# Kernel tuning notes

Hardware: AMD Instinct MI355X
Metric: run time of the kernel (lower is better)

## Reference

```python
import jax, jax.numpy as jnp
import numpy as np

SCALE = 100.0

def _build_tables():
    b2n = np.zeros((256, 32), np.float32)
    n2b = np.zeros((32, 256), np.float32)
    for byte in range(256):
        h, l = byte >> 4, byte & 15
        b2n[byte, h] = 1.0
        b2n[byte, 16 + l] = 1.0
        n2b[h, byte] = 1.0
        n2b[16 + l, byte] = 1.0
    add_table = np.zeros((16, 16, 2, 16), np.float32)
    carry_table = np.zeros((16, 16, 2, 2), np.float32)
    for x in range(16):
        for y in range(16):
            for c in range(2):
                t = x + y + c
                add_table[x, y, c, t % 16] = 1.0
                carry_table[x, y, c, t // 16] = 1.0
    return b2n, n2b, add_table, carry_table

def setup_inputs() -> dict:
    key = jax.random.key(0)
    k1, k2 = jax.random.split(key)
    B = 32768
    a = jax.random.normal(k1, (B, 4, 256), dtype=jnp.float32)
    b = jax.random.normal(k2, (B, 4, 256), dtype=jnp.float32)
    b2n, n2b, add_table, carry_table = _build_tables()
    return {"a": a, "b": b,
            "b2n": jnp.asarray(b2n), "n2b": jnp.asarray(n2b),
            "add_table": jnp.asarray(add_table), "carry_table": jnp.asarray(carry_table)}

def _byte_add_single(a, b, b2n, n2b, add_table, carry_table):
    # a, b: [4, 256]
    def to_nibbles(x):
        comb = x @ b2n  # [32]
        return jax.nn.softmax(comb[:16] * SCALE), jax.nn.softmax(comb[16:] * SCALE)

    def nibble_add(x, y, cin):
        # cin has shape [1] initially (broadcasts over carry axis, as torch einsum does) or [2]
        w = x[:, None, None] * y[None, :, None] * cin[None, None, :]
        w = jnp.broadcast_to(w, (16, 16, 2))
        s = jnp.einsum('ijk,ijkl->l', w, add_table)
        c = jnp.einsum('ijk,ijkl->l', w, carry_table)
        return jax.nn.softmax(s * SCALE), jax.nn.softmax(c * SCALE)

    def from_nibbles(h, l):
        return jax.nn.softmax((jnp.concatenate([h, l]) @ n2b) * SCALE)

    carry = jnp.ones((1,), a.dtype)  # matches torch.tensor([1.0]) initial carry
    outs = []
    for i in range(4):  # fixed 4-byte carry chain
        ah, al = to_nibbles(a[i])
        bh, bl = to_nibbles(b[i])
        sl, carry_out = nibble_add(al, bl, carry)
        sh, carry = nibble_add(ah, bh, carry_out)
        outs.append(from_nibbles(sh, sl))
    return jnp.stack(outs)  # [4, 256]

def reference(a, b, b2n, n2b, add_table, carry_table):
    f = jax.vmap(_byte_add_single, in_axes=(0, 0, None, None, None, None))
    return f(a, b, b2n, n2b, add_table, carry_table)  # [B, 4, 256]
```

## Files before the change

kernel.cpp:

```cpp
#include <hip/hip_runtime.h>
#include <cstddef>
#include <math.h>


__device__ __forceinline__ float exf(float t) {
  return (float)exp((double)t);
}

__device__ __forceinline__ void softmax16_np(const float* x, float* p) {
#pragma clang fp contract(off)
  float t[16];
#pragma unroll
  for (int j = 0; j < 16; ++j) t[j] = x[j] * 100.0f;
  float m = t[0];
#pragma unroll
  for (int j = 1; j < 16; ++j) m = fmaxf(m, t[j]);
  float e[16];
#pragma unroll
  for (int j = 0; j < 16; ++j) e[j] = exf(t[j] - m);
  float r0 = e[0] + e[8], r1 = e[1] + e[9], r2 = e[2] + e[10], r3 = e[3] + e[11];
  float r4 = e[4] + e[12], r5 = e[5] + e[13], r6 = e[6] + e[14], r7 = e[7] + e[15];
  float s = ((r0 + r1) + (r2 + r3)) + ((r4 + r5) + (r6 + r7));
#pragma unroll
  for (int j = 0; j < 16; ++j) p[j] = e[j] / s;
}

__device__ __forceinline__ void nibble_add_raw(const float* px, const float* py,
                                               float c0, float c1,
                                               float* s, float& n0, float& n1) {
#pragma clang fp contract(off)
  float ca = 0.f, cb = 0.f;
#pragma unroll
  for (int l = 0; l < 16; ++l) s[l] = 0.f;
#pragma unroll
  for (int i = 0; i < 16; ++i) {
#pragma unroll
    for (int j = 0; j < 16; ++j) {
      float wij = px[i] * py[j];
      float w0 = wij * c0;
      float w1 = wij * c1;
      const int t0 = i + j, t1 = i + j + 1;
      s[t0 & 15] += w0;
      if (t0 < 16) ca += w0; else cb += w0;
      s[t1 & 15] += w1;
      if (t1 < 16) ca += w1; else cb += w1;
    }
  }
  float u0 = ca * 100.0f, u1 = cb * 100.0f;
  float m = fmaxf(u0, u1);
  float e0 = exf(u0 - m), e1 = exf(u1 - m);
  float ss = e0 + e1;
  n0 = e0 / ss;
  n1 = e1 / ss;
}

extern "C" __global__ void __launch_bounds__(256, 1)
k1_prep(const float* __restrict__ A, const float* __restrict__ Bm,
        float* __restrict__ ws1, int nbatch) {
  __shared__ float buf[32][257];
  __shared__ float comb[32][33];
  const int tid = threadIdx.x;
  const int batch0 = blockIdx.x * 32;
  const int ib = blockIdx.y;
  const int inp = blockIdx.z;
  if (batch0 >= nbatch) return;
  const float* __restrict__ src =
      (inp == 0 ? A : Bm) + (size_t)batch0 * 1024 + ib * 256;

#pragma unroll
  for (int r = 0; r < 8; ++r) {
    int idx = r * 256 + tid;
    int row = idx >> 6, c4 = idx & 63;
    *(float4*)&buf[row][c4 * 4] = *(const float4*)(src + (size_t)row * 1024 + c4 * 4);
  }
  __syncthreads();

  {
#pragma clang fp contract(off)
    const int g = tid >> 5, bb = tid & 31;
    float acc[4] = {0.f, 0.f, 0.f, 0.f};
    if (g < 4) {
#pragma unroll
      for (int q = 0; q < 4; ++q) {
        float a = 0.f;
#pragma unroll
        for (int k4 = 0; k4 < 4; ++k4) {
          float4 v = *(const float4*)&buf[bb][(g * 4 + q) * 16 + k4 * 4];
          a += v.x; a += v.y; a += v.z; a += v.w;
        }
        acc[q] = a;
      }
#pragma unroll
      for (int q = 0; q < 4; ++q) comb[bb][g * 4 + q] = acc[q];
    } else {
      const int l0 = (g - 4) * 4;
#pragma unroll
      for (int m = 0; m < 16; ++m) {
        float4 v = *(const float4*)&buf[bb][m * 16 + l0];
        acc[0] += v.x; acc[1] += v.y; acc[2] += v.z; acc[3] += v.w;
      }
#pragma unroll
      for (int q = 0; q < 4; ++q) comb[bb][16 + l0 + q] = acc[q];
    }
  }
  __syncthreads();

  if (tid < 64) {
    const int nib = tid >> 5, bb = tid & 31;
    float x[16], p[16];
#pragma unroll
    for (int j = 0; j < 16; ++j) x[j] = comb[bb][nib * 16 + j];
    softmax16_np(x, p);
    const size_t r0 = (size_t)((ib * 2 + inp) * 32 + nib * 16);
#pragma unroll
    for (int j = 0; j < 16; ++j)
      ws1[(r0 + j) * nbatch + batch0 + bb] = p[j];
  }
}

__device__ __forceinline__ void k2_load(const float* __restrict__ ws1, int i,
                                        size_t batch, int nbatch, float* b) {
#pragma unroll
  for (int t = 0; t < 64; ++t)
    b[t] = ws1[(size_t)(i * 64 + t) * nbatch + batch];
}

__device__ __forceinline__ void k2_step(const float* b, float& cr0, float& cr1,
                                        float* __restrict__ ws2, int i,
                                        size_t batch, int nbatch) {
  float sl[16], sh[16], d0, d1;
  nibble_add_raw(b + 16, b + 48, cr0, cr1, sl, d0, d1);
  nibble_add_raw(b + 0,  b + 32, d0, d1, sh, cr0, cr1);
#pragma unroll
  for (int l = 0; l < 16; ++l) {
    ws2[(size_t)(i * 32 + l) * nbatch + batch] = sh[l];
    ws2[(size_t)(i * 32 + 16 + l) * nbatch + batch] = sl[l];
  }
}

extern "C" __global__ void __launch_bounds__(64, 1)
k2_chain(const float* __restrict__ ws1, float* __restrict__ ws2, int nbatch) {
  const size_t batch = (size_t)blockIdx.x * 64 + threadIdx.x;
  if (batch >= (size_t)nbatch) return;
  float cr0 = 1.0f, cr1 = 1.0f;
  float bufA[64], bufB[64];
  k2_load(ws1, 0, batch, nbatch, bufA);
  k2_load(ws1, 1, batch, nbatch, bufB);
  k2_step(bufA, cr0, cr1, ws2, 0, batch, nbatch);
  k2_load(ws1, 2, batch, nbatch, bufA);
  k2_step(bufB, cr0, cr1, ws2, 1, batch, nbatch);
  k2_load(ws1, 3, batch, nbatch, bufB);
  k2_step(bufA, cr0, cr1, ws2, 2, batch, nbatch);
  k2_step(bufB, cr0, cr1, ws2, 3, batch, nbatch);
}

extern "C" __global__ void __launch_bounds__(256, 1)
k3_out(const float* __restrict__ ws2, float* __restrict__ O, int nbatch) {
  __shared__ float pout[64][36];
  const int tid = threadIdx.x;
  const int batch0 = blockIdx.x * 64;
  const int ib = blockIdx.y;
  if (batch0 >= nbatch) return;

  if (tid < 128) {
    const int nib = tid >> 6, bb = tid & 63;
    float x[16], p[16], p2[16];
#pragma unroll
    for (int l = 0; l < 16; ++l)
      x[l] = ws2[(size_t)(ib * 32 + nib * 16 + l) * nbatch + batch0 + bb];
    softmax16_np(x, p);
    softmax16_np(p, p2);
#pragma unroll
    for (int j = 0; j < 16; ++j) pout[bb][nib * 20 + j] = p2[j];
  }
  __syncthreads();

#pragma unroll
  for (int kk = 0; kk < 16; ++kk) {
    int flat = kk * 1024 + tid * 4;
    int bb = flat >> 8;
    int b0 = flat & 255;
    float ph = pout[bb][b0 >> 4];
    int lo = 20 + (b0 & 15);
    float4 o;
    o.x = ph * pout[bb][lo + 0];
    o.y = ph * pout[bb][lo + 1];
    o.z = ph * pout[bb][lo + 2];
    o.w = ph * pout[bb][lo + 3];
    *(float4*)(O + ((size_t)(batch0 + bb) * 4 + ib) * 256 + b0) = o;
  }
}

__device__ __forceinline__ void nibble_add_np_fb(const float* px, const float* py,
                                                 float c0, float c1,
                                                 float* ps, float& n0, float& n1) {
  float s[16];
  nibble_add_raw(px, py, c0, c1, s, n0, n1);
  softmax16_np(s, ps);
}

__device__ __forceinline__ void buckets_np_fb(const float* __restrict__ row,
                                              float* hi, float* lo) {
#pragma clang fp contract(off)
#pragma unroll
  for (int j = 0; j < 16; ++j) { hi[j] = 0.f; lo[j] = 0.f; }
#pragma unroll
  for (int k4 = 0; k4 < 64; ++k4) {
    float4 x = *(const float4*)(row + k4 * 4);
    const int h = k4 >> 2, l0 = (k4 & 3) * 4;
    hi[h] += x.x;  hi[h] += x.y;  hi[h] += x.z;  hi[h] += x.w;
    lo[l0 + 0] += x.x;
    lo[l0 + 1] += x.y;
    lo[l0 + 2] += x.z;
    lo[l0 + 3] += x.w;
  }
}

extern "C" __global__ void __launch_bounds__(64, 1)
byteadd_fallback(const float* __restrict__ A, const float* __restrict__ Bm,
                 float* __restrict__ O, int nbatch) {
#pragma clang fp contract(off)
  const int b = blockIdx.x * 64 + threadIdx.x;
  if (b >= nbatch) return;
  const float* Ab = A + (size_t)b * 1024;
  const float* Bb = Bm + (size_t)b * 1024;
  float* Ob = O + (size_t)b * 1024;
  float cr0 = 1.0f, cr1 = 1.0f;
#pragma unroll 1
  for (int i = 0; i < 4; ++i) {
    float ah[16], al[16], bh[16], bl[16];
    buckets_np_fb(Ab + i * 256, ah, al);
    buckets_np_fb(Bb + i * 256, bh, bl);
    float pah[16], pal[16], pbh[16], pbl[16];
    softmax16_np(ah, pah);
    softmax16_np(al, pal);
    softmax16_np(bh, pbh);
    softmax16_np(bl, pbl);
    float psl[16], psh[16], d0, d1;
    nibble_add_np_fb(pal, pbl, cr0, cr1, psl, d0, d1);
    nibble_add_np_fb(pah, pbh, d0, d1, psh, cr0, cr1);
    float ph2[16], pl2[16];
    softmax16_np(psh, ph2);
    softmax16_np(psl, pl2);
#pragma unroll
    for (int k4 = 0; k4 < 64; ++k4) {
      const int h = k4 >> 2, l0 = (k4 & 3) * 4;
      const float ph = ph2[h];
      float4 o;
      o.x = ph * pl2[l0 + 0];
      o.y = ph * pl2[l0 + 1];
      o.z = ph * pl2[l0 + 2];
      o.w = ph * pl2[l0 + 3];
      *(float4*)(Ob + i * 256 + k4 * 4) = o;
    }
  }
}

extern "C" void kernel_launch(void* const* d_in, const int* in_sizes, int n_in,
                              void* d_out, int out_size, void* d_ws, size_t ws_size,
                              hipStream_t stream) {
  const float* A = (const float*)d_in[0];
  const float* B = (const float*)d_in[1];
  float* O = (float*)d_out;
  int nbatch = in_sizes[0] / 1024;
  size_t need = (size_t)384 * nbatch * sizeof(float);
  if (ws_size >= need && (nbatch & 63) == 0) {
    float* ws1 = (float*)d_ws;
    float* ws2 = ws1 + (size_t)256 * nbatch;
    k1_prep<<<dim3(nbatch / 32, 4, 2), dim3(256), 0, stream>>>(A, B, ws1, nbatch);
    k2_chain<<<dim3(nbatch / 64), dim3(64), 0, stream>>>(ws1, ws2, nbatch);
    k3_out<<<dim3(nbatch / 64, 4), dim3(256), 0, stream>>>(ws2, O, nbatch);
  } else {
    byteadd_fallback<<<dim3((nbatch + 63) / 64), dim3(64), 0, stream>>>(A, B, O, nbatch);
  }
}
```

Measured before the change: 197.1 us.

## Use one thread per batch row in prep kernel; process two bytes per output block

The prep kernel no longer stages 32 rows in shared memory and reduces them cooperatively. Each thread now reads its own 256-float row directly with float4 loads, accumulates the high and low nibble buckets in registers, and computes both softmaxes, so all 256 threads do work where only 64 did before. The output kernel now handles two bytes per block so every thread takes part in the softmax phase, and launch bounds are raised to allow more resident blocks. The trade is that the prep kernel's global reads are strided per thread (1024 floats apart) and no longer coalesced, and the fast path now requires the batch count to be a multiple of 256.

After: 282.0 us. 43.1% more time.

```diff
diff --git a/kernel.cpp b/kernel.cpp
--- a/kernel.cpp
+++ b/kernel.cpp
@@ -54,68 +54,45 @@
   n1 = e1 / ss;
 }
 
-extern "C" __global__ void __launch_bounds__(256, 1)
+extern "C" __global__ void __launch_bounds__(256, 4)
 k1_prep(const float* __restrict__ A, const float* __restrict__ Bm,
         float* __restrict__ ws1, int nbatch) {
-  __shared__ float buf[32][257];
-  __shared__ float comb[32][33];
-  const int tid = threadIdx.x;
-  const int batch0 = blockIdx.x * 32;
-  const int ib = blockIdx.y;
-  const int inp = blockIdx.z;
-  if (batch0 >= nbatch) return;
+#pragma clang fp contract(off)
+  const int batch = blockIdx.x * 256 + threadIdx.x;
+  if (batch >= nbatch) return;
+  const int ib = blockIdx.y, inp = blockIdx.z;
   const float* __restrict__ src =
-      (inp == 0 ? A : Bm) + (size_t)batch0 * 1024 + ib * 256;
-
-#pragma unroll
-  for (int r = 0; r < 8; ++r) {
-    int idx = r * 256 + tid;
-    int row = idx >> 6, c4 = idx & 63;
-    *(float4*)&buf[row][c4 * 4] = *(const float4*)(src + (size_t)row * 1024 + c4 * 4);
-  }
-  __syncthreads();
-
-  {
-#pragma clang fp contract(off)
-    const int g = tid >> 5, bb = tid & 31;
-    float acc[4] = {0.f, 0.f, 0.f, 0.f};
-    if (g < 4) {
-#pragma unroll
-      for (int q = 0; q < 4; ++q) {
-        float a = 0.f;
-#pragma unroll
-        for (int k4 = 0; k4 < 4; ++k4) {
-          float4 v = *(const float4*)&buf[bb][(g * 4 + q) * 16 + k4 * 4];
-          a += v.x; a += v.y; a += v.z; a += v.w;
-        }
-        acc[q] = a;
-      }
-#pragma unroll
-      for (int q = 0; q < 4; ++q) comb[bb][g * 4 + q] = acc[q];
-    } else {
-      const int l0 = (g - 4) * 4;
-#pragma unroll
-      for (int m = 0; m < 16; ++m) {
-        float4 v = *(const float4*)&buf[bb][m * 16 + l0];
-        acc[0] += v.x; acc[1] += v.y; acc[2] += v.z; acc[3] += v.w;
-      }
-#pragma unroll
-      for (int q = 0; q < 4; ++q) comb[bb][16 + l0 + q] = acc[q];
-    }
-  }
-  __syncthreads();
-
-  if (tid < 64) {
-    const int nib = tid >> 5, bb = tid & 31;
-    float x[16], p[16];
-#pragma unroll
-    for (int j = 0; j < 16; ++j) x[j] = comb[bb][nib * 16 + j];
-    softmax16_np(x, p);
-    const size_t r0 = (size_t)((ib * 2 + inp) * 32 + nib * 16);
-#pragma unroll
-    for (int j = 0; j < 16; ++j)
-      ws1[(r0 + j) * nbatch + batch0 + bb] = p[j];
-  }
+      (inp == 0 ? A : Bm) + (size_t)batch * 1024 + ib * 256;
+
+  float hi[16], lo[16];
+#pragma unroll
+  for (int j = 0; j < 16; ++j) { hi[j] = 0.f; lo[j] = 0.f; }
+#pragma unroll
+  for (int m = 0; m < 16; ++m) {
+    float4 v0 = *(const float4*)(src + m * 16 + 0);
+    float4 v1 = *(const float4*)(src + m * 16 + 4);
+    float4 v2 = *(const float4*)(src + m * 16 + 8);
+    float4 v3 = *(const float4*)(src + m * 16 + 12);
+    float a = hi[m];
+    a += v0.x; a += v0.y; a += v0.z; a += v0.w;
+    a += v1.x; a += v1.y; a += v1.z; a += v1.w;
+    a += v2.x; a += v2.y; a += v2.z; a += v2.w;
+    a += v3.x; a += v3.y; a += v3.z; a += v3.w;
+    hi[m] = a;
+    lo[0]  += v0.x; lo[1]  += v0.y; lo[2]  += v0.z; lo[3]  += v0.w;
+    lo[4]  += v1.x; lo[5]  += v1.y; lo[6]  += v1.z; lo[7]  += v1.w;
+    lo[8]  += v2.x; lo[9]  += v2.y; lo[10] += v2.z; lo[11] += v2.w;
+    lo[12] += v3.x; lo[13] += v3.y; lo[14] += v3.z; lo[15] += v3.w;
+  }
+
+  const size_t r0 = (size_t)((ib * 2 + inp) * 32);
+  float p[16];
+  softmax16_np(hi, p);
+#pragma unroll
+  for (int j = 0; j < 16; ++j) ws1[(r0 + j) * nbatch + batch] = p[j];
+  softmax16_np(lo, p);
+#pragma unroll
+  for (int j = 0; j < 16; ++j) ws1[(r0 + 16 + j) * nbatch + batch] = p[j];
 }
 
 __device__ __forceinline__ void k2_load(const float* __restrict__ ws1, int i,
@@ -154,40 +131,45 @@
   k2_step(bufB, cr0, cr1, ws2, 3, batch, nbatch);
 }
 
-extern "C" __global__ void __launch_bounds__(256, 1)
+extern "C" __global__ void __launch_bounds__(256, 2)
 k3_out(const float* __restrict__ ws2, float* __restrict__ O, int nbatch) {
-  __shared__ float pout[64][36];
+  __shared__ float pout[2][64][36];
   const int tid = threadIdx.x;
   const int batch0 = blockIdx.x * 64;
-  const int ib = blockIdx.y;
+  const int ib0 = blockIdx.y * 2;
   if (batch0 >= nbatch) return;
 
-  if (tid < 128) {
-    const int nib = tid >> 6, bb = tid & 63;
+  {
+    const int ibl = tid >> 7;
+    const int nib = (tid >> 6) & 1;
+    const int bb = tid & 63;
     float x[16], p[16], p2[16];
 #pragma unroll
     for (int l = 0; l < 16; ++l)
-      x[l] = ws2[(size_t)(ib * 32 + nib * 16 + l) * nbatch + batch0 + bb];
+      x[l] = ws2[(size_t)((ib0 + ibl) * 32 + nib * 16 + l) * nbatch + batch0 + bb];
     softmax16_np(x, p);
     softmax16_np(p, p2);
 #pragma unroll
-    for (int j = 0; j < 16; ++j) pout[bb][nib * 20 + j] = p2[j];
+    for (int j = 0; j < 16; ++j) pout[ibl][bb][nib * 20 + j] = p2[j];
   }
   __syncthreads();
 
 #pragma unroll
-  for (int kk = 0; kk < 16; ++kk) {
-    int flat = kk * 1024 + tid * 4;
-    int bb = flat >> 8;
-    int b0 = flat & 255;
-    float ph = pout[bb][b0 >> 4];
-    int lo = 20 + (b0 & 15);
-    float4 o;
-    o.x = ph * pout[bb][lo + 0];
-    o.y = ph * pout[bb][lo + 1];
-    o.z = ph * pout[bb][lo + 2];
-    o.w = ph * pout[bb][lo + 3];
-    *(float4*)(O + ((size_t)(batch0 + bb) * 4 + ib) * 256 + b0) = o;
+  for (int ibl = 0; ibl < 2; ++ibl) {
+#pragma unroll
+    for (int kk = 0; kk < 16; ++kk) {
+      int flat = kk * 1024 + tid * 4;
+      int bb = flat >> 8;
+      int b0 = flat & 255;
+      float ph = pout[ibl][bb][b0 >> 4];
+      int lo = 20 + (b0 & 15);
+      float4 o;
+      o.x = ph * pout[ibl][bb][lo + 0];
+      o.y = ph * pout[ibl][bb][lo + 1];
+      o.z = ph * pout[ibl][bb][lo + 2];
+      o.w = ph * pout[ibl][bb][lo + 3];
+      *(float4*)(O + ((size_t)(batch0 + bb) * 4 + ib0 + ibl) * 256 + b0) = o;
+    }
   }
 }
 
@@ -264,12 +246,12 @@
   float* O = (float*)d_out;
   int nbatch = in_sizes[0] / 1024;
   size_t need = (size_t)384 * nbatch * sizeof(float);
-  if (ws_size >= need && (nbatch & 63) == 0) {
+  if (ws_size >= need && (nbatch & 255) == 0) {
     float* ws1 = (float*)d_ws;
     float* ws2 = ws1 + (size_t)256 * nbatch;
-    k1_prep<<<dim3(nbatch / 32, 4, 2), dim3(256), 0, stream>>>(A, B, ws1, nbatch);
+    k1_prep<<<dim3(nbatch / 256, 4, 2), dim3(256), 0, stream>>>(A, B, ws1, nbatch);
     k2_chain<<<dim3(nbatch / 64), dim3(64), 0, stream>>>(ws1, ws2, nbatch);
-    k3_out<<<dim3(nbatch / 64, 4), dim3(256), 0, stream>>>(ws2, O, nbatch);
+    k3_out<<<dim3(nbatch / 64, 2), dim3(256), 0, stream>>>(ws2, O, nbatch);
   } else {
     byteadd_fallback<<<dim3((nbatch + 63) / 64), dim3(64), 0, stream>>>(A, B, O, nbatch);
   }
```

## Raise occupancy of prep/output kernels and process two bytes per k3 block

Applied to the files above, without the earlier changes.

Changes launch bounds of k1_prep and k3_out from 1 to 4 blocks per CU, and pads the k1 shared buffer differently while having each wave load full rows. The k1 reduction now reads scalars from shared memory instead of float4 vectors. k3_out now handles two byte positions per block, so all 256 threads do softmax work and the grid is halved. The aim is better latency hiding and fewer idle threads, at the cost of more shared memory per k3 block and a possible change in LDS bank conflicts.

Result: no change. 196.6 us (-0.2%).

```diff
diff --git a/kernel.cpp b/kernel.cpp
--- a/kernel.cpp
+++ b/kernel.cpp
@@ -54,59 +54,55 @@
   n1 = e1 / ss;
 }
 
-extern "C" __global__ void __launch_bounds__(256, 1)
+extern "C" __global__ void __launch_bounds__(256, 4)
 k1_prep(const float* __restrict__ A, const float* __restrict__ Bm,
         float* __restrict__ ws1, int nbatch) {
-  __shared__ float buf[32][257];
+#pragma clang fp contract(off)
+  __shared__ float buf[32][261];
   __shared__ float comb[32][33];
   const int tid = threadIdx.x;
+  const int wave = tid >> 6, lane = tid & 63;
   const int batch0 = blockIdx.x * 32;
-  const int ib = blockIdx.y;
-  const int inp = blockIdx.z;
+  const int ib = blockIdx.y, inp = blockIdx.z;
   if (batch0 >= nbatch) return;
   const float* __restrict__ src =
       (inp == 0 ? A : Bm) + (size_t)batch0 * 1024 + ib * 256;
 
 #pragma unroll
-  for (int r = 0; r < 8; ++r) {
-    int idx = r * 256 + tid;
-    int row = idx >> 6, c4 = idx & 63;
-    *(float4*)&buf[row][c4 * 4] = *(const float4*)(src + (size_t)row * 1024 + c4 * 4);
+  for (int it = 0; it < 8; ++it) {
+    const int bb = it * 4 + wave;
+    *(float4*)&buf[bb][lane * 4] =
+        *(const float4*)(src + (size_t)bb * 1024 + lane * 4);
   }
   __syncthreads();
 
   {
-#pragma clang fp contract(off)
-    const int g = tid >> 5, bb = tid & 31;
-    float acc[4] = {0.f, 0.f, 0.f, 0.f};
+    const int g = tid >> 5;
+    const int bb = tid & 31;
     if (g < 4) {
 #pragma unroll
       for (int q = 0; q < 4; ++q) {
+        const int u = g * 4 + q;
         float a = 0.f;
 #pragma unroll
-        for (int k4 = 0; k4 < 4; ++k4) {
-          float4 v = *(const float4*)&buf[bb][(g * 4 + q) * 16 + k4 * 4];
-          a += v.x; a += v.y; a += v.z; a += v.w;
-        }
-        acc[q] = a;
+        for (int e = 0; e < 16; ++e) a += buf[bb][u * 16 + e];
+        comb[bb][u] = a;
       }
-#pragma unroll
-      for (int q = 0; q < 4; ++q) comb[bb][g * 4 + q] = acc[q];
     } else {
-      const int l0 = (g - 4) * 4;
-#pragma unroll
-      for (int m = 0; m < 16; ++m) {
-        float4 v = *(const float4*)&buf[bb][m * 16 + l0];
-        acc[0] += v.x; acc[1] += v.y; acc[2] += v.z; acc[3] += v.w;
+#pragma unroll
+      for (int q = 0; q < 4; ++q) {
+        const int l = (g - 4) * 4 + q;
+        float a = 0.f;
+#pragma unroll
+        for (int m = 0; m < 16; ++m) a += buf[bb][m * 16 + l];
+        comb[bb][16 + l] = a;
       }
-#pragma unroll
-      for (int q = 0; q < 4; ++q) comb[bb][16 + l0 + q] = acc[q];
     }
   }
   __syncthreads();
 
   if (tid < 64) {
-    const int nib = tid >> 5, bb = tid & 31;
+    const int bb = tid & 31, nib = tid >> 5;
     float x[16], p[16];
 #pragma unroll
     for (int j = 0; j < 16; ++j) x[j] = comb[bb][nib * 16 + j];
@@ -154,40 +150,45 @@
   k2_step(bufB, cr0, cr1, ws2, 3, batch, nbatch);
 }
 
-extern "C" __global__ void __launch_bounds__(256, 1)
+extern "C" __global__ void __launch_bounds__(256, 4)
 k3_out(const float* __restrict__ ws2, float* __restrict__ O, int nbatch) {
-  __shared__ float pout[64][36];
+  __shared__ float pout[2][64][36];
   const int tid = threadIdx.x;
   const int batch0 = blockIdx.x * 64;
-  const int ib = blockIdx.y;
+  const int ib0 = blockIdx.y * 2;
   if (batch0 >= nbatch) return;
 
-  if (tid < 128) {
-    const int nib = tid >> 6, bb = tid & 63;
+  {
+    const int ibl = tid >> 7;
+    const int nib = (tid >> 6) & 1;
+    const int bb = tid & 63;
     float x[16], p[16], p2[16];
 #pragma unroll
     for (int l = 0; l < 16; ++l)
-      x[l] = ws2[(size_t)(ib * 32 + nib * 16 + l) * nbatch + batch0 + bb];
+      x[l] = ws2[(size_t)((ib0 + ibl) * 32 + nib * 16 + l) * nbatch + batch0 + bb];
     softmax16_np(x, p);
     softmax16_np(p, p2);
 #pragma unroll
-    for (int j = 0; j < 16; ++j) pout[bb][nib * 20 + j] = p2[j];
+    for (int j = 0; j < 16; ++j) pout[ibl][bb][nib * 20 + j] = p2[j];
   }
   __syncthreads();
 
 #pragma unroll
-  for (int kk = 0; kk < 16; ++kk) {
-    int flat = kk * 1024 + tid * 4;
-    int bb = flat >> 8;
-    int b0 = flat & 255;
-    float ph = pout[bb][b0 >> 4];
-    int lo = 20 + (b0 & 15);
-    float4 o;
-    o.x = ph * pout[bb][lo + 0];
-    o.y = ph * pout[bb][lo + 1];
-    o.z = ph * pout[bb][lo + 2];
-    o.w = ph * pout[bb][lo + 3];
-    *(float4*)(O + ((size_t)(batch0 + bb) * 4 + ib) * 256 + b0) = o;
+  for (int ibl = 0; ibl < 2; ++ibl) {
+#pragma unroll
+    for (int kk = 0; kk < 16; ++kk) {
+      int flat = kk * 1024 + tid * 4;
+      int bb = flat >> 8;
+      int b0 = flat & 255;
+      float ph = pout[ibl][bb][b0 >> 4];
+      int lo = 20 + (b0 & 15);
+      float4 o;
+      o.x = ph * pout[ibl][bb][lo + 0];
+      o.y = ph * pout[ibl][bb][lo + 1];
+      o.z = ph * pout[ibl][bb][lo + 2];
+      o.w = ph * pout[ibl][bb][lo + 3];
+      *(float4*)(O + ((size_t)(batch0 + bb) * 4 + ib0 + ibl) * 256 + b0) = o;
+    }
   }
 }
 
@@ -269,7 +270,7 @@
     float* ws2 = ws1 + (size_t)256 * nbatch;
     k1_prep<<<dim3(nbatch / 32, 4, 2), dim3(256), 0, stream>>>(A, B, ws1, nbatch);
     k2_chain<<<dim3(nbatch / 64), dim3(64), 0, stream>>>(ws1, ws2, nbatch);
-    k3_out<<<dim3(nbatch / 64, 4), dim3(256), 0, stream>>>(ws2, O, nbatch);
+    k3_out<<<dim3(nbatch / 64, 2), dim3(256), 0, stream>>>(ws2, O, nbatch);
   } else {
     byteadd_fallback<<<dim3((nbatch + 63) / 64), dim3(64), 0, stream>>>(A, B, O, nbatch);
   }
```
